# Kernel tuning notes

Hardware: AMD Instinct MI355X
Metric: run time of the kernel (lower is better)

Reference implementation:

```python
import jax, jax.numpy as jnp
import numpy as np


def conv2d(x, w, b):
    # x: [B,C,H,W], w: [O,I,5,5], VALID, stride 1 (matches torch Conv2d defaults)
    y = jax.lax.conv_general_dilated(x, w, (1, 1), 'VALID',
                                     dimension_numbers=('NCHW', 'OIHW', 'NCHW'))
    return y + b[None, :, None, None]


def maxpool_2x5(x):
    # MaxPool2d(kernel=(2,5), stride=(2,1))
    return jax.lax.reduce_window(x, -jnp.inf, jax.lax.max,
                                 (1, 1, 2, 5), (1, 1, 2, 1), 'VALID')


def gru(x, w_ih, w_hh, b_ih, b_hh):
    # Faithful torch nn.GRU (batch_first=False): x is [L, N, 64]; gate order r,z,n.
    H = w_hh.shape[1]
    h0 = jnp.zeros((x.shape[1], H), x.dtype)

    def step(h, xt):
        gi = xt @ w_ih.T + b_ih
        gh = h @ w_hh.T + b_hh
        i_r, i_z, i_n = jnp.split(gi, 3, axis=-1)
        h_r, h_z, h_n = jnp.split(gh, 3, axis=-1)
        r = jax.nn.sigmoid(i_r + h_r)
        z = jax.nn.sigmoid(i_z + h_z)
        n = jnp.tanh(i_n + r * h_n)
        h_new = (1.0 - z) * n + z * h
        return h_new, h_new

    _, ys = jax.lax.scan(step, h0, x)
    return ys


def branch(x, w1, b1, w2, b2, w3, b3, lw, lb, gwih, gwhh, gbih, gbhh):
    x = x[:, None]                      # [B,1,H,W]
    x = conv2d(x, w1, b1)
    x = conv2d(x, w2, b2)
    x = conv2d(x, w3, b3)
    x = maxpool_2x5(x)                  # [B,64,58,W']
    B = x.shape[0]
    x = x.reshape(B, x.shape[-1], 3712)  # same row-major reshape as torch
    x = x @ lw.T + lb                   # [B,W',64]
    # nn.GRU without batch_first scans over dim 0 (batch!) — replicate exactly
    return gru(x, gwih, gwhh, gbih, gbhh)


def _make_params(key):
    ks = iter(jax.random.split(key, 40))
    def p(shape, scale=0.05):
        return (jax.random.normal(next(ks), shape, jnp.float32) * scale)
    d = {}
    for pre in ('e', 't'):
        d[f'{pre}_w1'] = p((16, 1, 5, 5)); d[f'{pre}_b1'] = p((16,))
        d[f'{pre}_w2'] = p((32, 16, 5, 5)); d[f'{pre}_b2'] = p((32,))
        d[f'{pre}_w3'] = p((64, 32, 5, 5)); d[f'{pre}_b3'] = p((64,))
        d[f'{pre}l_w'] = p((64, 3712), 0.01); d[f'{pre}l_b'] = p((64,))
        d[f'{pre}g_wih'] = p((192, 64)); d[f'{pre}g_whh'] = p((192, 64))
        d[f'{pre}g_bih'] = p((192,)); d[f'{pre}g_bhh'] = p((192,))
    d['a_w'] = p((1, 64)); d['a_b'] = p((1,))
    d['h_w'] = p((128, 64)); d['h_b'] = p((128,))
    d['c_w'] = p((2, 128)); d['c_b'] = p((2,))
    return d


def setup_inputs() -> dict:
    key = jax.random.key(0)
    k1, k2, k3 = jax.random.split(key, 3)
    inp = {
        'evaluation': jax.random.normal(k1, (4, 128, 2048), jnp.float32),
        'template': jax.random.normal(k2, (4, 128, 1040), jnp.float32),
    }
    inp.update(_make_params(k3))
    return inp


def reference(evaluation, template,
              e_w1, e_b1, e_w2, e_b2, e_w3, e_b3, el_w, el_b,
              eg_wih, eg_whh, eg_bih, eg_bhh,
              t_w1, t_b1, t_w2, t_b2, t_w3, t_b3, tl_w, tl_b,
              tg_wih, tg_whh, tg_bih, tg_bhh,
              a_w, a_b, h_w, h_b, c_w, c_b):
    e = branch(evaluation, e_w1, e_b1, e_w2, e_b2, e_w3, e_b3,
               el_w, el_b, eg_wih, eg_whh, eg_bih, eg_bhh)   # [B,Se,64]
    t = branch(template, t_w1, t_b1, t_w2, t_b2, t_w3, t_b3,
               tl_w, tl_b, tg_wih, tg_whh, tg_bih, tg_bhh)   # [B,St,64]
    # bmm(template, eval^T) -> [B,St,Se], softmax over Se
    tt = jax.nn.softmax(jnp.einsum('btd,bed->bte', t, e), axis=-1)
    # bmm(tt^T, template) -> [B,Se,64]
    tt = jnp.einsum('bte,btd->bed', tt, t)
    tt = jnp.abs(tt - e)
    # attention over eval sequence positions
    att = jax.nn.softmax((e @ a_w.T + a_b)[..., 0], axis=-1)  # [B,Se]
    # vectorized form of the original Python double loop
    red = jnp.einsum('bed,be->bd', tt, att)                   # [B,64]
    h = jax.nn.relu(red @ h_w.T + h_b)
    return jax.nn.softmax(h @ c_w.T + c_b, axis=-1)           # [B,2]
```

## Files before the change

### kernel.cpp

```cpp
#include <hip/hip_runtime.h>
#include <hip/hip_bf16.h>
#include <cmath>


typedef unsigned short u16;
typedef unsigned int u32;
typedef __attribute__((ext_vector_type(8))) short bf16x8;
typedef __attribute__((ext_vector_type(8))) unsigned short u16x8;
typedef __attribute__((ext_vector_type(16))) float f32x16;

__device__ __forceinline__ u16 f2bf(float f) {
  unsigned int x = __float_as_uint(f);
  return (u16)((x + 0x7fffu + ((x >> 16) & 1u)) >> 16);
}
__device__ __forceinline__ float bf2f(u16 v) {
  return __uint_as_float(((unsigned int)v) << 16);
}
__device__ __forceinline__ u32 f2bf_pk(float a, float b) {
  __hip_bfloat162 h = __float22bfloat162_rn(float2{a, b});
  u32 r;
  __builtin_memcpy(&r, &h, 4);
  return r;
}

static const size_t OFF_BEFF_E  = 0;
static const size_t OFF_BEFF_T  = 64;
static const size_t OFF_BIAS2_E = 128;
static const size_t OFF_BIAS2_T = 320;
static const size_t OFF_WKX_E   = 512;
static const size_t OFF_WKX_T   = 27136;
static const size_t OFF_W12P_E  = 53760;
static const size_t OFF_W12P_T  = 63008;
static const size_t OFF_B12_E   = 72256;
static const size_t OFF_B12_T   = 72288;
static const size_t OFF_LWT1_E  = 72320;
static const size_t OFF_LWT1_T  = 191104;
static const size_t OFF_ATT     = 309888;
static const size_t OFF_XYBF_E  = 318016;
static const size_t OFF_XYBF_T  = 578112;
static const size_t OFF_TTBF    = 709184;
static const size_t OFF_LIN_E   = 840256;
static const size_t OFF_LIN_T   = 1360448;
static const size_t OFF_RED     = 1622592;
static const size_t OFF_RSUM    = 1622848;
static const size_t ZERO_F4     = 196672;
static const size_t ZSTRIDE     = 372;
static const size_t OFF_ATTW    = 1626944;
static const size_t OFF_GI_E    = 2147136;
static const size_t OFF_GI_T    = 3707712;

__global__ __launch_bounds__(320) void prep_kernel(
    const float* __restrict__ w1e, const float* __restrict__ b1e,
    const float* __restrict__ w2e, const float* __restrict__ b2e,
    const float* __restrict__ w1t, const float* __restrict__ b1t,
    const float* __restrict__ w2t, const float* __restrict__ b2t,
    float* __restrict__ w12p_e, float* __restrict__ w12p_t,
    float* __restrict__ b12o_e, float* __restrict__ b12o_t,
    const float* __restrict__ wih_e, const float* __restrict__ bih_e,
    const float* __restrict__ lb_e, float* __restrict__ bias2_e,
    const float* __restrict__ wih_t, const float* __restrict__ bih_t,
    const float* __restrict__ lb_t, float* __restrict__ bias2_t,
    const float* __restrict__ lwe, const float* __restrict__ lwt,
    u16* __restrict__ lwt1_e, u16* __restrict__ lwt1_t,
    float4* __restrict__ zbase) {
  const int bx = blockIdx.x;
  const int tid = threadIdx.x;
  {
    const size_t base = (size_t)bx * ZSTRIDE;
    const float4 z = {0.f, 0.f, 0.f, 0.f};
    for (size_t i = base + tid; i < base + ZSTRIDE && i < ZERO_F4; i += 320)
      zbase[i] = z;
  }
  if (bx >= 66) {
    if (tid < 256) {
      const int k = bx - 66;
      const int br = k / 232, j = k - br * 232;
      const float* src = br ? lwt : lwe;
      u16* dst = br ? lwt1_t : lwt1_e;
      const int e = j * 1024 + tid * 4;
      const int h = e >> 12;
      const int rem = e & 4095;
      const int n = rem >> 6, c = rem & 63;
      const float* s = src + (size_t)n * 3712 + (size_t)c * 58 + h;
      const float v0 = s[0], v1 = s[58], v2 = s[116], v3 = s[174];
      *(u32*)&dst[e] = f2bf_pk(v0, v1);
      *(u32*)&dst[e + 2] = f2bf_pk(v2, v3);
    }
    return;
  }
  if (bx >= 64) {
    const int br = bx - 64;
    const float* wih = br ? wih_t : wih_e;
    const float* bih = br ? bih_t : bih_e;
    const float* lb = br ? lb_t : lb_e;
    float* bias2 = br ? bias2_t : bias2_e;
    __shared__ float s_lb[64];
    if (tid < 64) s_lb[tid] = lb[tid];
    __syncthreads();
    if (tid < 192) {
      float acc = bih[tid];
      const float* wr = wih + tid * 64;
      for (int d = 0; d < 64; ++d) acc = fmaf(wr[d], s_lb[d], acc);
      bias2[tid] = acc;
    }
    return;
  }
  const int br = bx >> 5;
  const float* w1 = br ? w1t : w1e;
  const float* b1 = br ? b1t : b1e;
  const float* w2 = br ? w2t : w2e;
  const float* b2 = br ? b2t : b2e;
  float* w12p = br ? w12p_t : w12p_e;
  float* b12o = br ? b12o_t : b12o_e;
  const int c12 = bx & 31;
  __shared__ float s_w1pad[16 * 169];
  __shared__ float s_w2c[400];
  __shared__ float s_b1[16];
  for (int i = tid; i < 2704; i += 320) s_w1pad[i] = 0.f;
  if (tid < 16) s_b1[tid] = b1[tid];
  __syncthreads();
  for (int i = tid; i < 400; i += 320) {
    const int c1 = i / 25, r = (i % 25) / 5, cc = i % 5;
    s_w1pad[c1 * 169 + (r + 4) * 13 + (cc + 4)] = w1[i];
    s_w2c[i] = w2[c12 * 400 + i];
  }
  __syncthreads();
  if (tid < 289) {
    const int py = tid / 17, px = tid % 17;
    float v = 0.f;
    if (py >= 4 && py <= 12 && px >= 4 && px <= 12) {
      const int sy = py - 4, sx = px - 4;
      float accs[2] = {0.f, 0.f};
// ... 170 lines not shown
#pragma unroll
        for (int ks = 0; ks < 4; ++ks) bb[ks] = *(const bf16x8*)(bp2 + ks * 16);
      }
      f32x16 c0a = {}, c1a = {}, c0b = {}, c1b = {};
      const u16* bxp = s_x + g8;
#pragma unroll
      for (int kx = 0; kx < 6; ++kx) {
        bf16x8 b0 = *(const bf16x8*)(bxp + (l31 + kx) * 24);
        bf16x8 b1 = *(const bf16x8*)(bxp + (32 + l31 + kx) * 24);
        bf16x8 b0q = *(const bf16x8*)(bxp + (l31 + kx + 7) * 24);
        bf16x8 b1q = *(const bf16x8*)(bxp + (32 + l31 + kx + 7) * 24);
        c0a = __builtin_amdgcn_mfma_f32_32x32x16_bf16(wfrag[kx], b0, c0a, 0, 0, 0);
        c1a = __builtin_amdgcn_mfma_f32_32x32x16_bf16(wfrag[kx], b1, c1a, 0, 0, 0);
        c0b = __builtin_amdgcn_mfma_f32_32x32x16_bf16(wfrag[kx + 7], b0q, c0b, 0, 0, 0);
        c1b = __builtin_amdgcn_mfma_f32_32x32x16_bf16(wfrag[kx + 7], b1q, c1b, 0, 0, 0);
      }
      {
        bf16x8 b0 = *(const bf16x8*)(bxp + (l31 + 6) * 24);
        bf16x8 b1 = *(const bf16x8*)(bxp + (32 + l31 + 6) * 24);
        c0a = __builtin_amdgcn_mfma_f32_32x32x16_bf16(wfrag[6], b0, c0a, 0, 0, 0);
        c1a = __builtin_amdgcn_mfma_f32_32x32x16_bf16(wfrag[6], b1, c1a, 0, 0, 0);
      }
#pragma unroll
      for (int r = 0; r < 16; ++r) {
        const int c = cm + (r & 3) + 8 * (r >> 2) + (g8 >> 1);
        u16* o = s_out + (rsel * 64 + c) * 72;
        const u32 pk = f2bf_pk(c0a[r] + c0b[r], c1a[r] + c1b[r]);
        o[l31] = (u16)pk;
        o[32 + l31] = (u16)(pk >> 16);
      }
      __syncthreads();
      {
        const int pc = tid & 63, tg = tid >> 6;
        const int t0 = tg * 16;
        const float bias = s_beff[pc];
        const u16* r0p = s_out + pc * 72 + t0;
        const u16* r1p = s_out + (64 + pc) * 72 + t0;
        const u16x8 a0 = *(const u16x8*)(r0p);
        const u16x8 a1 = *(const u16x8*)(r0p + 8);
        const u16x8 a2 = *(const u16x8*)(r0p + 16);
        const u16x8 q0 = *(const u16x8*)(r1p);
        const u16x8 q1 = *(const u16x8*)(r1p + 8);
        const u16x8 q2 = *(const u16x8*)(r1p + 16);
        float m01[20];
#pragma unroll
        for (int j = 0; j < 8; ++j) {
          m01[j] = fmaxf(bf2f(a0[j]), bf2f(q0[j]));
          m01[j + 8] = fmaxf(bf2f(a1[j]), bf2f(q1[j]));
          if (j < 4) m01[j + 16] = fmaxf(bf2f(a2[j]), bf2f(q2[j]));
        }
#pragma unroll
        for (int i = 0; i < 16; ++i) {
          if (t0 + i < 60) {
            float m = m01[i];
#pragma unroll
            for (int k = 1; k < 5; ++k) m = fmaxf(m, m01[i + k]);
            s_poolT[(t0 + i) * 72 + pc] = f2bf(m + bias);
          }
        }
      }
      __syncthreads();
      {
        const u16* ap2 = s_poolT + (th + l31) * 72 + g8;
#pragma unroll
        for (int ks = 0; ks < 4; ++ks) {
          bf16x8 a = *(const bf16x8*)(ap2 + ks * 16);
          accL = __builtin_amdgcn_mfma_f32_32x32x16_bf16(a, bb[ks], accL, 0, 0, 0);
        }
      }
    }
  }
  {
    const int nn = nh + l31;
#pragma unroll
    for (int r = 0; r < 16; ++r) {
      const int t = th + (r & 3) + 8 * (r >> 2) + (g8 >> 1);
      const int tt = cb + t;
      if (t < 60 && tt < T)
        atomicAdd(&lin[((size_t)b * T + tt) * 64 + nn], accL[r]);
    }
  }
}

__global__ __launch_bounds__(256) void gemm_gi_kernel(
    const float* __restrict__ Ae, const float* __restrict__ Wte,
    const float* __restrict__ biase, float* __restrict__ oute,
    const float* __restrict__ At, const float* __restrict__ Wtt,
    const float* __restrict__ biast, float* __restrict__ outt) {
  const int bx = blockIdx.x;
  const bool ev = bx < 127;
  const float* A = ev ? Ae : At;
  const float* Wt = ev ? Wte : Wtt;
  const float* bias = ev ? biase : biast;
  float* out = ev ? oute : outt;
  const int r0 = (ev ? bx : bx - 127) * 64;
  const int N = 192, K = 64;
  __shared__ float sA[64 * 33];
  __shared__ float sB[64 * 33];
  const int tid = threadIdx.x;
  const int n0 = blockIdx.y * 64;
  const int ty = tid >> 4, tx = tid & 15;
  float acc[4][4] = {};
  for (int kc = 0; kc < K; kc += 32) {
    __syncthreads();
#pragma unroll
    for (int rep = 0; rep < 8; ++rep) {
      const int l = tid + rep * 256;
      const int row = l >> 5, kk = l & 31;
      sA[row * 33 + kk] = A[(size_t)(r0 + row) * K + kc + kk];
      sB[row * 33 + kk] = Wt[(size_t)(n0 + row) * K + kc + kk];
    }
    __syncthreads();
#pragma unroll 8
    for (int kk = 0; kk < 32; ++kk) {
      const float a0 = sA[(ty * 4 + 0) * 33 + kk];
      const float a1 = sA[(ty * 4 + 1) * 33 + kk];
      const float a2 = sA[(ty * 4 + 2) * 33 + kk];
      const float a3 = sA[(ty * 4 + 3) * 33 + kk];
      const float b0 = sB[(tx * 4 + 0) * 33 + kk];
      const float b1 = sB[(tx * 4 + 1) * 33 + kk];
      const float b2 = sB[(tx * 4 + 2) * 33 + kk];
      const float b3 = sB[(tx * 4 + 3) * 33 + kk];
      acc[0][0] = fmaf(a0, b0, acc[0][0]); acc[0][1] = fmaf(a0, b1, acc[0][1]);
      acc[0][2] = fmaf(a0, b2, acc[0][2]); acc[0][3] = fmaf(a0, b3, acc[0][3]);
      acc[1][0] = fmaf(a1, b0, acc[1][0]); acc[1][1] = fmaf(a1, b1, acc[1][1]);
      acc[1][2] = fmaf(a1, b2, acc[1][2]); acc[1][3] = fmaf(a1, b3, acc[1][3]);
      acc[2][0] = fmaf(a2, b0, acc[2][0]); acc[2][1] = fmaf(a2, b1, acc[2][1]);
      acc[2][2] = fmaf(a2, b2, acc[2][2]); acc[2][3] = fmaf(a2, b3, acc[2][3]);
      acc[3][0] = fmaf(a3, b0, acc[3][0]); acc[3][1] = fmaf(a3, b1, acc[3][1]);
      acc[3][2] = fmaf(a3, b2, acc[3][2]); acc[3][3] = fmaf(a3, b3, acc[3][3]);
    }
  }
#pragma unroll
  for (int i = 0; i < 4; ++i)
#pragma unroll
    for (int j = 0; j < 4; ++j)
      out[(size_t)(r0 + ty * 4 + i) * N + n0 + tx * 4 + j] =
          acc[i][j] + bias[n0 + tx * 4 + j];
}

__global__ __launch_bounds__(256) void gru_rec_kernel(
    float* __restrict__ xyE, const float* __restrict__ giE,
    const float* __restrict__ whhE, const float* __restrict__ bhhE,
    float* __restrict__ xyT, const float* __restrict__ giT,
    const float* __restrict__ whhT, const float* __restrict__ bhhT,
    u16* __restrict__ xybfE, u16* __restrict__ xybfT, u16* __restrict__ ttbf,
    const float* __restrict__ a_w, const float* __restrict__ a_b,
    float* __restrict__ logits) {
  const int bxid = blockIdx.x;
  const bool ev = bxid < 127;
  float* xy = ev ? xyE : xyT;
  u16* xybf = ev ? xybfE : xybfT;
  const float* gi = ev ? giE : giT;
  const float* whh = ev ? whhE : whhT;
  const float* bhh = ev ? bhhE : bhhT;
  const int T = ev ? 2032 : 1024;
  const int t0 = (ev ? bxid : bxid - 127) * 16;
  __shared__ float s_whh_t[64 * 192];
  __shared__ float s_h[16][64];
  __shared__ float s_aw[64];
  const int tid = threadIdx.x;
  const int lane = tid & 63, wave = tid >> 6;
  for (int i = tid; i < 192 * 64; i += 256) {
    const int j = i >> 6, d = i & 63;
    s_whh_t[d * 192 + j] = whh[i];
  }
  for (int i = tid; i < 16 * 64; i += 256) (&s_h[0][0])[i] = 0.f;
  if (tid < 64) s_aw[tid] = a_w[tid];
  const float ab = a_b[0];
  const float bhr = bhh[lane], bhz = bhh[64 + lane], bhn = bhh[128 + lane];
  __syncthreads();
  for (int b = 0; b < 4; ++b) {
    float gir[4], giz[4], gin[4];
#pragma unroll
    for (int sl = 0; sl < 4; ++sl) {
      int t = t0 + wave * 4 + sl; if (t > T - 1) t = T - 1;
      const float* girow = gi + ((size_t)b * T + t) * 192;
      gir[sl] = girow[lane]; giz[sl] = girow[64 + lane]; gin[sl] = girow[128 + lane];
    }
    float ahr[4] = {}, ahz[4] = {}, ahn[4] = {};
    for (int d = 0; d < 64; ++d) {
      const float wr_ = s_whh_t[d * 192 + lane];
      const float wz_ = s_whh_t[d * 192 + 64 + lane];
      const float wn_ = s_whh_t[d * 192 + 128 + lane];
#pragma unroll
      for (int sl = 0; sl < 4; ++sl) {
        const float hv = s_h[wave * 4 + sl][d];
        ahr[sl] = fmaf(wr_, hv, ahr[sl]);
        ahz[sl] = fmaf(wz_, hv, ahz[sl]);
        ahn[sl] = fmaf(wn_, hv, ahn[sl]);
      }
    }
    float hn[4];
#pragma unroll
    for (int sl = 0; sl < 4; ++sl) {
      const float r = 1.f / (1.f + __expf(-(gir[sl] + ahr[sl] + bhr)));
      const float z = 1.f / (1.f + __expf(-(giz[sl] + ahz[sl] + bhz)));
      const float n = tanhf(gin[sl] + r * (ahn[sl] + bhn));
      hn[sl] = (1.f - z) * n + z * s_h[wave * 4 + sl][lane];
    }
    __syncthreads();
#pragma unroll
    for (int sl = 0; sl < 4; ++sl) {
      const int t = t0 + wave * 4 + sl;
      s_h[wave * 4 + sl][lane] = hn[sl];
      if (t < T) {
        const size_t idx = ((size_t)b * T + t) * 64 + lane;
        xy[idx] = hn[sl];
        xybf[idx] = f2bf(hn[sl]);
        if (ev) {
          float v = hn[sl] * s_aw[lane];
#pragma unroll
          for (int off = 32; off > 0; off >>= 1) v += __shfl_down(v, off, 64);
          if (lane == 0) logits[b * 2032 + t] = v + ab;
        } else {
          ttbf[((size_t)b * 64 + lane) * 1024 + t] = f2bf(hn[sl]);
        }
      }
    }
    __syncthreads();
  }
}

__global__ __launch_bounds__(256) void rowsum_kernel(
    const u16* __restrict__ tbf, const u16* __restrict__ ebf,
    float* __restrict__ rowsum) {
  __shared__ __align__(16) u16 sA[64 * 72];
  __shared__ __align__(16) u16 sB[128 * 72];
  const int tid = threadIdx.x;
  const int b = blockIdx.z;
  const int tau0 = blockIdx.x * 64;
  const int e0 = blockIdx.y * 128;
  const int lane = tid & 63, wave = tid >> 6;
  const int l31 = lane & 31, g8 = (lane >> 5) * 8;
  {
    const int row = tid >> 2, seg = (tid & 3) * 16;
    const u16* ap = &tbf[((size_t)b * 1024 + tau0 + row) * 64 + seg];
    u16* da = &sA[row * 72 + seg];
    *(u16x8*)da = *(const u16x8*)ap;
    *(u16x8*)(da + 8) = *(const u16x8*)(ap + 8);
  }
#pragma unroll
  for (int r = 0; r < 4; ++r) {
    const int q = tid + r * 256;
    const int row = q >> 3, seg = (q & 7) * 8;
    int eps = e0 + row; if (eps > 2031) eps = 2031;
    *(u16x8*)&sB[row * 72 + seg] =
        *(const u16x8*)&ebf[((size_t)b * 2032 + eps) * 64 + seg];
  }
  __syncthreads();
  const int mh = (wave & 1) * 32;
  const int nq = (wave >> 1) * 64;
  f32x16 acc0 = {}, acc1 = {};
#pragma unroll
  for (int ks = 0; ks < 4; ++ks) {
    bf16x8 a = *(const bf16x8*)&sA[(mh + l31) * 72 + ks * 16 + g8];
    bf16x8 b0 = *(const bf16x8*)&sB[(nq + l31) * 72 + ks * 16 + g8];
    bf16x8 b1 = *(const bf16x8*)&sB[(nq + 32 + l31) * 72 + ks * 16 + g8];
    acc0 = __builtin_amdgcn_mfma_f32_32x32x16_bf16(a, b0, acc0, 0, 0, 0);
    acc1 = __builtin_amdgcn_mfma_f32_32x32x16_bf16(a, b1, acc1, 0, 0, 0);
  }
  const int ep0 = e0 + nq + l31;
  const int ep1 = ep0 + 32;
#pragma unroll
  for (int r = 0; r < 16; ++r) {
    const int tau = tau0 + mh + (r & 3) + 8 * (r >> 2) + (g8 >> 1);
    float part = 0.f;
    if (ep0 < 2032) part += __expf(acc0[r]);
    if (ep1 < 2032) part += __expf(acc1[r]);
#pragma unroll
    for (int off = 16; off > 0; off >>= 1) part += __shfl_down(part, off, 32);
    if (l31 == 0) atomicAdd(&rowsum[b * 1024 + tau], part);
  }
}

__global__ __launch_bounds__(256) void att_softmax_kernel(
    const float* __restrict__ logits, float* __restrict__ attw) {
  __shared__ float s_att[2032];
  __shared__ float sred[4];
  const int tid = threadIdx.x;
  const int lane = tid & 63, wave = tid >> 6;
  const int b = blockIdx.x;
  float m = -3.4e38f;
  for (int i = tid; i < 2032; i += 256) {
    const float v = logits[b * 2032 + i];
    s_att[i] = v;
    m = fmaxf(m, v);
  }
#pragma unroll
  for (int off = 32; off > 0; off >>= 1) m = fmaxf(m, __shfl_down(m, off, 64));
  if (lane == 0) sred[wave] = m;
  __syncthreads();
  m = fmaxf(fmaxf(sred[0], sred[1]), fmaxf(sred[2], sred[3]));
  __syncthreads();
  float ssum = 0.f;
  for (int i = tid; i < 2032; i += 256) {
    const float v = __expf(s_att[i] - m);
    s_att[i] = v;
    ssum += v;
  }
#pragma unroll
  for (int off = 32; off > 0; off >>= 1) ssum += __shfl_down(ssum, off, 64);
  if (lane == 0) sred[wave] = ssum;
  __syncthreads();
  const float inv = 1.f / (sred[0] + sred[1] + sred[2] + sred[3]);
  for (int i = tid; i < 2032; i += 256) attw[b * 2032 + i] = s_att[i] * inv;
}

__global__ __launch_bounds__(256) void pv_red_kernel(
    const u16* __restrict__ tbf, const u16* __restrict__ ebf,
    const u16* __restrict__ ttbf, const float* __restrict__ rowsum,
    const float* __restrict__ attw, const float* __restrict__ emat,
    float* __restrict__ red) {
  __shared__ __align__(16) u16 sE[64 * 72];
  __shared__ __align__(16) u16 sT[64 * 72];
  __shared__ __align__(16) u16 sTT[64 * 72];
  __shared__ __align__(16) u16 sPT[64 * 72];
  __shared__ float s_rs[64];
  __shared__ float s_att[64];
  __shared__ float s_part[4][32];
  const int tid = threadIdx.x;
  const int b = blockIdx.y;
  const int e0 = blockIdx.x * 64;
  const int lane = tid & 63, wave = tid >> 6;
  const int l31 = lane & 31, g8 = (lane >> 5) * 8;
  const int mh = (wave & 1) * 32;
  const int nh = (wave >> 1) * 32;
  {
    const int row = tid >> 2, seg = (tid & 3) * 16;
    int eps = e0 + row; if (eps > 2031) eps = 2031;
    const u16* ap = &ebf[((size_t)b * 2032 + eps) * 64 + seg];
    u16* da = &sE[row * 72 + seg];
    *(u16x8*)da = *(const u16x8*)ap;
    *(u16x8*)(da + 8) = *(const u16x8*)(ap + 8);
  }
  if (tid < 64) {
    const int e = e0 + tid;
    s_att[tid] = (e < 2032) ? attw[b * 2032 + e] : 0.f;
  }
  f32x16 accPV = {};
  for (int ch = 0; ch < 16; ++ch) {
    const int tc = ch * 64;
    __syncthreads();
    {
      const int row = tid >> 2, seg = (tid & 3) * 16;
      const u16* ap = &tbf[((size_t)b * 1024 + tc + row) * 64 + seg];
      u16* da = &sT[row * 72 + seg];
      *(u16x8*)da = *(const u16x8*)ap;
      *(u16x8*)(da + 8) = *(const u16x8*)(ap + 8);
    }
#pragma unroll
    for (int k = 0; k < 2; ++k) {
      const int q = tid + k * 256;
      const int row = q >> 3, seg = (q & 7) * 8;
      *(u16x8*)&sTT[row * 72 + seg] =
          *(const u16x8*)&ttbf[((size_t)b * 64 + row) * 1024 + tc + seg];
    }
    if (tid < 64) s_rs[tid] = 1.0f / rowsum[b * 1024 + tc + tid];
    __syncthreads();
    f32x16 acc = {};
#pragma unroll
    for (int ks = 0; ks < 4; ++ks) {
      bf16x8 a = *(const bf16x8*)&sT[(mh + l31) * 72 + ks * 16 + g8];
      bf16x8 bb = *(const bf16x8*)&sE[(nh + l31) * 72 + ks * 16 + g8];
      acc = __builtin_amdgcn_mfma_f32_32x32x16_bf16(a, bb, acc, 0, 0, 0);
    }
#pragma unroll
    for (int r = 0; r < 16; ++r) {
      const int tl = mh + (r & 3) + 8 * (r >> 2) + (g8 >> 1);
      const int el = nh + l31;
      sPT[el * 72 + tl] = f2bf(__expf(acc[r]) * s_rs[tl]);
    }
    __syncthreads();
#pragma unroll
    for (int ks = 0; ks < 4; ++ks) {
      bf16x8 a = *(const bf16x8*)&sPT[(mh + l31) * 72 + ks * 16 + g8];
      bf16x8 bb = *(const bf16x8*)&sTT[(nh + l31) * 72 + ks * 16 + g8];
      accPV = __builtin_amdgcn_mfma_f32_32x32x16_bf16(a, bb, accPV, 0, 0, 0);
    }
  }
  float local = 0.f;
#pragma unroll
  for (int r = 0; r < 16; ++r) {
    const int el = mh + (r & 3) + 8 * (r >> 2) + (g8 >> 1);
    const int eps = e0 + el;
    if (eps < 2032) {
      const size_t idx = ((size_t)b * 2032 + eps) * 64 + nh + l31;
      local = fmaf(fabsf(accPV[r] - emat[idx]), s_att[el], local);
    }
  }
  local += __shfl_xor(local, 32, 64);
  if (lane < 32) s_part[wave][lane] = local;
  __syncthreads();
  if (tid < 64) {
    const int d = tid;
    const float v = (d < 32) ? (s_part[0][d] + s_part[1][d])
                             : (s_part[2][d - 32] + s_part[3][d - 32]);
    atomicAdd(&red[b * 64 + d], v);
  }
}

__global__ __launch_bounds__(128) void mlp_kernel(
    const float* __restrict__ red, const float* __restrict__ h_w,
    const float* __restrict__ h_b, const float* __restrict__ c_w,
    const float* __restrict__ c_b, float* __restrict__ out) {
  __shared__ float s_red[64];
  __shared__ float s_hv[128];
  const int tid = threadIdx.x;
  const int b = blockIdx.x;
  if (tid < 64) s_red[tid] = red[b * 64 + tid];
  __syncthreads();
  {
    float acc = h_b[tid];
    const float* hw = h_w + tid * 64;
    for (int d = 0; d < 64; ++d) acc = fmaf(s_red[d], hw[d], acc);
    s_hv[tid] = fmaxf(acc, 0.f);
  }
  __syncthreads();
  if (tid == 0) {
    float l0 = c_b[0], l1 = c_b[1];
    for (int j = 0; j < 128; ++j) {
      l0 = fmaf(s_hv[j], c_w[j], l0);
      l1 = fmaf(s_hv[j], c_w[128 + j], l1);
    }
    const float mm = fmaxf(l0, l1);
    const float e0 = __expf(l0 - mm), e1 = __expf(l1 - mm);
    const float invs = 1.f / (e0 + e1);
    out[b * 2 + 0] = e0 * invs;
    out[b * 2 + 1] = e1 * invs;
  }
}

extern "C" void kernel_launch(void* const* d_in, const int* in_sizes, int n_in,
                              void* d_out, int out_size, void* d_ws, size_t ws_size,
                              hipStream_t stream) {
  const float* evaluation = (const float*)d_in[0];
  const float* templ      = (const float*)d_in[1];
  const float* e_w1 = (const float*)d_in[2];
  const float* e_b1 = (const float*)d_in[3];
  const float* e_w2 = (const float*)d_in[4];
  const float* e_b2 = (const float*)d_in[5];
  const float* e_w3 = (const float*)d_in[6];
  const float* e_b3 = (const float*)d_in[7];
  const float* el_w = (const float*)d_in[8];
  const float* el_b = (const float*)d_in[9];
  const float* eg_wih = (const float*)d_in[10];
  const float* eg_whh = (const float*)d_in[11];
  const float* eg_bih = (const float*)d_in[12];
  const float* eg_bhh = (const float*)d_in[13];
  const float* t_w1 = (const float*)d_in[14];
  const float* t_b1 = (const float*)d_in[15];
  const float* t_w2 = (const float*)d_in[16];
  const float* t_b2 = (const float*)d_in[17];
  const float* t_w3 = (const float*)d_in[18];
  const float* t_b3 = (const float*)d_in[19];
  const float* tl_w = (const float*)d_in[20];
  const float* tl_b = (const float*)d_in[21];
  const float* tg_wih = (const float*)d_in[22];
  const float* tg_whh = (const float*)d_in[23];
  const float* tg_bih = (const float*)d_in[24];
  const float* tg_bhh = (const float*)d_in[25];
  const float* a_w = (const float*)d_in[26];
  const float* a_b = (const float*)d_in[27];
  const float* h_w = (const float*)d_in[28];
  const float* h_b = (const float*)d_in[29];
  const float* c_w = (const float*)d_in[30];
  const float* c_b = (const float*)d_in[31];

  float* ws = (float*)d_ws;
  float* beff_e  = ws + OFF_BEFF_E;
  float* beff_t  = ws + OFF_BEFF_T;
  float* bias2_e = ws + OFF_BIAS2_E;
  float* bias2_t = ws + OFF_BIAS2_T;
  u16*   wkx_e   = (u16*)(ws + OFF_WKX_E);
  u16*   wkx_t   = (u16*)(ws + OFF_WKX_T);
  float* w12p_e  = ws + OFF_W12P_E;
  float* w12p_t  = ws + OFF_W12P_T;
  float* b12_e   = ws + OFF_B12_E;
  float* b12_t   = ws + OFF_B12_T;
  u16*   lwt1_e  = (u16*)(ws + OFF_LWT1_E);
  u16*   lwt1_t  = (u16*)(ws + OFF_LWT1_T);
  float* attbuf  = ws + OFF_ATT;
  u16*   xybf_e  = (u16*)(ws + OFF_XYBF_E);
  u16*   xybf_t  = (u16*)(ws + OFF_XYBF_T);
  u16*   ttbf    = (u16*)(ws + OFF_TTBF);
  float* lin_e   = ws + OFF_LIN_E;
  float* lin_t   = ws + OFF_LIN_T;
  float* redbuf  = ws + OFF_RED;
  float* rsum    = ws + OFF_RSUM;
  float* attw    = ws + OFF_ATTW;
  float* gi_e    = ws + OFF_GI_E;
  float* gi_t    = ws + OFF_GI_T;

  prep_kernel<<<530, 320, 0, stream>>>(
      e_w1, e_b1, e_w2, e_b2, t_w1, t_b1, t_w2, t_b2, w12p_e, w12p_t, b12_e, b12_t,
      eg_wih, eg_bih, el_b, bias2_e, tg_wih, tg_bih, tl_b, bias2_t,
      el_w, tl_w, lwt1_e, lwt1_t, (float4*)lin_e);
  compose_weff_kernel<<<dim3(64, 2), 256, 0, stream>>>(
      e_w3, e_b3, t_w3, t_b3, w12p_e, w12p_t, b12_e, b12_t, wkx_e, wkx_t, beff_e, beff_t);

  conv_pool_lin_kernel<<<dim3(34, 10, 8), 256, 0, stream>>>(
      evaluation, wkx_e, beff_e, lwt1_e, lin_e,
      templ, wkx_t, beff_t, lwt1_t, lin_t);
  gemm_gi_kernel<<<dim3(191, 3), 256, 0, stream>>>(
      lin_e, eg_wih, bias2_e, gi_e, lin_t, tg_wih, bias2_t, gi_t);
  gru_rec_kernel<<<191, 256, 0, stream>>>(
      lin_e, gi_e, eg_whh, eg_bhh, lin_t, gi_t, tg_whh, tg_bhh,
      xybf_e, xybf_t, ttbf, a_w, a_b, attbuf);

  rowsum_kernel<<<dim3(16, 16, 4), 256, 0, stream>>>(xybf_t, xybf_e, rsum);
  att_softmax_kernel<<<4, 256, 0, stream>>>(attbuf, attw);
  pv_red_kernel<<<dim3(32, 4), 256, 0, stream>>>(
      xybf_t, xybf_e, ttbf, rsum, attw, lin_e, redbuf);

  mlp_kernel<<<4, 128, 0, stream>>>(redbuf, h_w, h_b, c_w, c_b, (float*)d_out);
}
```

Before: 307.2 us.

## Fuse attention softmax and MLP into pv_red kernel, split D across blocks

Removes the separate attention-softmax and MLP kernels. Each pv_red block recomputes the softmax max and sum over the 2032 logits itself, and the last block to finish (tracked by an atomic counter) runs the final MLP. The grid gains a z dimension that splits the 64 output features into two halves, and the second GEMM's K dimension is split across waves and merged through shared memory. Loads of the next T/TT/rowsum chunk are prefetched into registers. In exchange, every block redundantly reads the full logits row and depends on a zeroed counter in the workspace (ZERO_F4 shifted to cover it).

```diff
diff --git a/kernel.cpp b/kernel.cpp
--- a/kernel.cpp
+++ b/kernel.cpp
@@ -43,9 +43,9 @@
 static const size_t OFF_LIN_T   = 1360448;
 static const size_t OFF_RED     = 1622592;
 static const size_t OFF_RSUM    = 1622848;
-static const size_t ZERO_F4     = 196672;
+static const size_t OFF_CNT     = 1626944;
+static const size_t ZERO_F4     = 196673;
 static const size_t ZSTRIDE     = 372;
-static const size_t OFF_ATTW    = 1626944;
 static const size_t OFF_GI_E    = 2147136;
 static const size_t OFF_GI_T    = 3707712;
 
@@ -576,58 +576,33 @@
   }
 }
 
-__global__ __launch_bounds__(256) void att_softmax_kernel(
-    const float* __restrict__ logits, float* __restrict__ attw) {
-  __shared__ float s_att[2032];
-  __shared__ float sred[4];
-  const int tid = threadIdx.x;
-  const int lane = tid & 63, wave = tid >> 6;
-  const int b = blockIdx.x;
-  float m = -3.4e38f;
-  for (int i = tid; i < 2032; i += 256) {
-    const float v = logits[b * 2032 + i];
-    s_att[i] = v;
-    m = fmaxf(m, v);
-  }
-#pragma unroll
-  for (int off = 32; off > 0; off >>= 1) m = fmaxf(m, __shfl_down(m, off, 64));
-  if (lane == 0) sred[wave] = m;
-  __syncthreads();
-  m = fmaxf(fmaxf(sred[0], sred[1]), fmaxf(sred[2], sred[3]));
-  __syncthreads();
-  float ssum = 0.f;
-  for (int i = tid; i < 2032; i += 256) {
-    const float v = __expf(s_att[i] - m);
-    s_att[i] = v;
-    ssum += v;
-  }
-#pragma unroll
-  for (int off = 32; off > 0; off >>= 1) ssum += __shfl_down(ssum, off, 64);
-  if (lane == 0) sred[wave] = ssum;
-  __syncthreads();
-  const float inv = 1.f / (sred[0] + sred[1] + sred[2] + sred[3]);
-  for (int i = tid; i < 2032; i += 256) attw[b * 2032 + i] = s_att[i] * inv;
-}
-
 __global__ __launch_bounds__(256) void pv_red_kernel(
     const u16* __restrict__ tbf, const u16* __restrict__ ebf,
     const u16* __restrict__ ttbf, const float* __restrict__ rowsum,
-    const float* __restrict__ attw, const float* __restrict__ emat,
-    float* __restrict__ red) {
+    const float* __restrict__ logits, const float* __restrict__ emat,
+    float* __restrict__ red, float* __restrict__ cnt,
+    const float* __restrict__ h_w, const float* __restrict__ h_b,
+    const float* __restrict__ c_w, const float* __restrict__ c_b,
+    float* __restrict__ out) {
   __shared__ __align__(16) u16 sE[64 * 72];
   __shared__ __align__(16) u16 sT[64 * 72];
-  __shared__ __align__(16) u16 sTT[64 * 72];
+  __shared__ __align__(16) u16 sTT[32 * 72];
   __shared__ __align__(16) u16 sPT[64 * 72];
   __shared__ float s_rs[64];
   __shared__ float s_att[64];
-  __shared__ float s_part[4][32];
+  __shared__ float s_red4[4];
+  __shared__ float s_merge[2][32 * 33];
+  __shared__ float s_ep[2][32];
+  __shared__ int s_last;
   const int tid = threadIdx.x;
   const int b = blockIdx.y;
   const int e0 = blockIdx.x * 64;
+  const int dh = blockIdx.z;
   const int lane = tid & 63, wave = tid >> 6;
   const int l31 = lane & 31, g8 = (lane >> 5) * 8;
   const int mh = (wave & 1) * 32;
-  const int nh = (wave >> 1) * 32;
+  const int kh = wave >> 1;
+  const int nh = kh * 32;
   {
     const int row = tid >> 2, seg = (tid & 3) * 16;
     int eps = e0 + row; if (eps > 2031) eps = 2031;
@@ -636,29 +611,57 @@
     *(u16x8*)da = *(const u16x8*)ap;
     *(u16x8*)(da + 8) = *(const u16x8*)(ap + 8);
   }
-  if (tid < 64) {
-    const int e = e0 + tid;
-    s_att[tid] = (e < 2032) ? attw[b * 2032 + e] : 0.f;
+  {
+    float m = -3.4e38f;
+    for (int i = tid; i < 2032; i += 256) m = fmaxf(m, logits[b * 2032 + i]);
+#pragma unroll
+    for (int off = 32; off > 0; off >>= 1) m = fmaxf(m, __shfl_down(m, off, 64));
+    if (lane == 0) s_red4[wave] = m;
+    __syncthreads();
+    m = fmaxf(fmaxf(s_red4[0], s_red4[1]), fmaxf(s_red4[2], s_red4[3]));
+    __syncthreads();
+    float ssum = 0.f;
+    for (int i = tid; i < 2032; i += 256) ssum += __expf(logits[b * 2032 + i] - m);
+#pragma unroll
+    for (int off = 32; off > 0; off >>= 1) ssum += __shfl_down(ssum, off, 64);
+    if (lane == 0) s_red4[wave] = ssum;
+    __syncthreads();
+    const float inv = 1.f / (s_red4[0] + s_red4[1] + s_red4[2] + s_red4[3]);
+    if (tid < 64) {
+      const int e = e0 + tid;
+      s_att[tid] = (e < 2032) ? __expf(logits[b * 2032 + e] - m) * inv : 0.f;
+    }
+  }
+  u16x8 pT0, pT1, pTT;
+  float pRS = 1.f;
+  {
+    const int row = tid >> 2, seg = (tid & 3) * 16;
+    const u16* ap = &tbf[((size_t)b * 1024 + row) * 64 + seg];
+    pT0 = *(const u16x8*)ap; pT1 = *(const u16x8*)(ap + 8);
+    const int r2 = tid >> 3, s2 = (tid & 7) * 8;
+    pTT = *(const u16x8*)&ttbf[((size_t)b * 64 + dh * 32 + r2) * 1024 + s2];
+    if (tid < 64) pRS = rowsum[b * 1024 + tid];
   }
   f32x16 accPV = {};
   for (int ch = 0; ch < 16; ++ch) {
-    const int tc = ch * 64;
     __syncthreads();
     {
       const int row = tid >> 2, seg = (tid & 3) * 16;
+      u16* da = &sT[row * 72 + seg];
+      *(u16x8*)da = pT0; *(u16x8*)(da + 8) = pT1;
+      const int r2 = tid >> 3, s2 = (tid & 7) * 8;
+      *(u16x8*)&sTT[r2 * 72 + s2] = pTT;
+      if (tid < 64) s_rs[tid] = 1.0f / pRS;
+    }
+    if (ch + 1 < 16) {
+      const int tc = (ch + 1) * 64;
+      const int row = tid >> 2, seg = (tid & 3) * 16;
       const u16* ap = &tbf[((size_t)b * 1024 + tc + row) * 64 + seg];
-      u16* da = &sT[row * 72 + seg];
-      *(u16x8*)da = *(const u16x8*)ap;
-      *(u16x8*)(da + 8) = *(const u16x8*)(ap + 8);
-    }
-#pragma unroll
-    for (int k = 0; k < 2; ++k) {
-      const int q = tid + k * 256;
-      const int row = q >> 3, seg = (q & 7) * 8;
-      *(u16x8*)&sTT[row * 72 + seg] =
-          *(const u16x8*)&ttbf[((size_t)b * 64 + row) * 1024 + tc + seg];
-    }
-    if (tid < 64) s_rs[tid] = 1.0f / rowsum[b * 1024 + tc + tid];
+      pT0 = *(const u16x8*)ap; pT1 = *(const u16x8*)(ap + 8);
+      const int r2 = tid >> 3, s2 = (tid & 7) * 8;
+      pTT = *(const u16x8*)&ttbf[((size_t)b * 64 + dh * 32 + r2) * 1024 + tc + s2];
+      if (tid < 64) pRS = rowsum[b * 1024 + tc + tid];
+    }
     __syncthreads();
     f32x16 acc = {};
 #pragma unroll
@@ -675,61 +678,72 @@
     }
     __syncthreads();
 #pragma unroll
-    for (int ks = 0; ks < 4; ++ks) {
+    for (int kq = 0; kq < 2; ++kq) {
+      const int ks = kh * 2 + kq;
       bf16x8 a = *(const bf16x8*)&sPT[(mh + l31) * 72 + ks * 16 + g8];
-      bf16x8 bb = *(const bf16x8*)&sTT[(nh + l31) * 72 + ks * 16 + g8];
+      bf16x8 bb = *(const bf16x8*)&sTT[l31 * 72 + ks * 16 + g8];
       accPV = __builtin_amdgcn_mfma_f32_32x32x16_bf16(a, bb, accPV, 0, 0, 0);
     }
   }
-  float local = 0.f;
-#pragma unroll
-  for (int r = 0; r < 16; ++r) {
-    const int el = mh + (r & 3) + 8 * (r >> 2) + (g8 >> 1);
-    const int eps = e0 + el;
-    if (eps < 2032) {
-      const size_t idx = ((size_t)b * 2032 + eps) * 64 + nh + l31;
-      local = fmaf(fabsf(accPV[r] - emat[idx]), s_att[el], local);
-    }
-  }
-  local += __shfl_xor(local, 32, 64);
-  if (lane < 32) s_part[wave][lane] = local;
   __syncthreads();
-  if (tid < 64) {
-    const int d = tid;
-    const float v = (d < 32) ? (s_part[0][d] + s_part[1][d])
-                             : (s_part[2][d - 32] + s_part[3][d - 32]);
-    atomicAdd(&red[b * 64 + d], v);
-  }
-}
-
-__global__ __launch_bounds__(128) void mlp_kernel(
-    const float* __restrict__ red, const float* __restrict__ h_w,
-    const float* __restrict__ h_b, const float* __restrict__ c_w,
-    const float* __restrict__ c_b, float* __restrict__ out) {
-  __shared__ float s_red[64];
-  __shared__ float s_hv[128];
-  const int tid = threadIdx.x;
-  const int b = blockIdx.x;
-  if (tid < 64) s_red[tid] = red[b * 64 + tid];
+  if (kh == 1) {
+#pragma unroll
+    for (int r = 0; r < 16; ++r) {
+      const int row = (r & 3) + 8 * (r >> 2) + (g8 >> 1);
+      s_merge[wave & 1][row * 33 + l31] = accPV[r];
+    }
+  }
   __syncthreads();
-  {
-    float acc = h_b[tid];
-    const float* hw = h_w + tid * 64;
-    for (int d = 0; d < 64; ++d) acc = fmaf(s_red[d], hw[d], acc);
-    s_hv[tid] = fmaxf(acc, 0.f);
+  if (kh == 0) {
+    float local = 0.f;
+#pragma unroll
+    for (int r = 0; r < 16; ++r) {
+      const int row = (r & 3) + 8 * (r >> 2) + (g8 >> 1);
+      const float pv = accPV[r] + s_merge[wave & 1][row * 33 + l31];
+      const int eps = e0 + mh + row;
+      if (eps < 2032) {
+        const size_t idx = ((size_t)b * 2032 + eps) * 64 + dh * 32 + l31;
+        local = fmaf(fabsf(pv - emat[idx]), s_att[mh + row], local);
+      }
+    }
+    local += __shfl_xor(local, 32, 64);
+    if (lane < 32) s_ep[wave & 1][lane] = local;
   }
   __syncthreads();
+  if (tid < 32)
+    atomicAdd(&red[b * 64 + dh * 32 + tid], s_ep[0][tid] + s_ep[1][tid]);
+  __threadfence();
   if (tid == 0) {
-    float l0 = c_b[0], l1 = c_b[1];
-    for (int j = 0; j < 128; ++j) {
-      l0 = fmaf(s_hv[j], c_w[j], l0);
-      l1 = fmaf(s_hv[j], c_w[128 + j], l1);
-    }
-    const float mm = fmaxf(l0, l1);
-    const float e0 = __expf(l0 - mm), e1 = __expf(l1 - mm);
-    const float invs = 1.f / (e0 + e1);
-    out[b * 2 + 0] = e0 * invs;
-    out[b * 2 + 1] = e1 * invs;
+    const float old = atomicAdd(cnt, 1.0f);
+    s_last = (old > 254.5f) ? 1 : 0;
+  }
+  __syncthreads();
+  if (s_last) {
+    __threadfence();
+    for (int bq = 0; bq < 4; ++bq) {
+      if (tid < 64) s_rs[tid] = red[bq * 64 + tid];
+      __syncthreads();
+      if (tid < 128) {
+        float accq = h_b[tid];
+        const float* hw = h_w + tid * 64;
+        for (int dd = 0; dd < 64; ++dd) accq = fmaf(s_rs[dd], hw[dd], accq);
+        s_merge[0][tid] = fmaxf(accq, 0.f);
+      }
+      __syncthreads();
+      if (tid == 0) {
+        float l0 = c_b[0], l1 = c_b[1];
+        for (int j = 0; j < 128; ++j) {
+          l0 = fmaf(s_merge[0][j], c_w[j], l0);
+          l1 = fmaf(s_merge[0][j], c_w[128 + j], l1);
+        }
+        const float mm = fmaxf(l0, l1);
+        const float e0v = __expf(l0 - mm), e1v = __expf(l1 - mm);
+        const float invs = 1.f / (e0v + e1v);
+        out[bq * 2 + 0] = e0v * invs;
+        out[bq * 2 + 1] = e1v * invs;
+      }
+      __syncthreads();
+    }
   }
 }
 
@@ -790,7 +804,7 @@
   float* lin_t   = ws + OFF_LIN_T;
   float* redbuf  = ws + OFF_RED;
   float* rsum    = ws + OFF_RSUM;
-  float* attw    = ws + OFF_ATTW;
+  float* cntbuf  = ws + OFF_CNT;
   float* gi_e    = ws + OFF_GI_E;
   float* gi_t    = ws + OFF_GI_T;
 
@@ -811,9 +825,7 @@
       xybf_e, xybf_t, ttbf, a_w, a_b, attbuf);
 
   rowsum_kernel<<<dim3(16, 16, 4), 256, 0, stream>>>(xybf_t, xybf_e, rsum);
-  att_softmax_kernel<<<4, 256, 0, stream>>>(attbuf, attw);
-  pv_red_kernel<<<dim3(32, 4), 256, 0, stream>>>(
-      xybf_t, xybf_e, ttbf, rsum, attw, lin_e, redbuf);
-
-  mlp_kernel<<<4, 128, 0, stream>>>(redbuf, h_w, h_b, c_w, c_b, (float*)d_out);
-}
+  pv_red_kernel<<<dim3(32, 4, 2), 256, 0, stream>>>(
+      xybf_t, xybf_e, ttbf, rsum, attbuf, lin_e, redbuf, cntbuf,
+      h_w, h_b, c_w, c_b, (float*)d_out);
+}
```

Measured after the change: 319.3 us. 3.9% more time.

## Fuse GRU input-gate GEMM into the recurrence kernel

Applied to the files above, without the earlier changes.

Removes the separate gemm_gi_kernel and its global gi buffers. The GRU recurrence kernel now stages W_ih and the combined bias in LDS. It loads each step's linear-layer rows into shared memory and accumulates the input gates alongside the hidden-gate dot products in the same d-loop. This saves one launch and the multi-megabyte write and re-read of the gate pre-activations. In exchange, LDS use roughly doubles and the per-step inner loop carries twice the FMA and shared-memory load work.

```diff
diff --git a/kernel.cpp b/kernel.cpp
--- a/kernel.cpp
+++ b/kernel.cpp
@@ -46,8 +46,6 @@
 static const size_t ZERO_F4     = 196672;
 static const size_t ZSTRIDE     = 372;
 static const size_t OFF_ATTW    = 1626944;
-static const size_t OFF_GI_E    = 2147136;
-static const size_t OFF_GI_T    = 3707712;
 
 __global__ __launch_bounds__(320) void prep_kernel(
     const float* __restrict__ w1e, const float* __restrict__ b1e,
@@ -384,68 +382,13 @@
   }
 }
 
-__global__ __launch_bounds__(256) void gemm_gi_kernel(
-    const float* __restrict__ Ae, const float* __restrict__ Wte,
-    const float* __restrict__ biase, float* __restrict__ oute,
-    const float* __restrict__ At, const float* __restrict__ Wtt,
-    const float* __restrict__ biast, float* __restrict__ outt) {
-  const int bx = blockIdx.x;
-  const bool ev = bx < 127;
-  const float* A = ev ? Ae : At;
-  const float* Wt = ev ? Wte : Wtt;
-  const float* bias = ev ? biase : biast;
-  float* out = ev ? oute : outt;
-  const int r0 = (ev ? bx : bx - 127) * 64;
-  const int N = 192, K = 64;
-  __shared__ float sA[64 * 33];
-  __shared__ float sB[64 * 33];
-  const int tid = threadIdx.x;
-  const int n0 = blockIdx.y * 64;
-  const int ty = tid >> 4, tx = tid & 15;
-  float acc[4][4] = {};
-  for (int kc = 0; kc < K; kc += 32) {
-    __syncthreads();
-#pragma unroll
-    for (int rep = 0; rep < 8; ++rep) {
-      const int l = tid + rep * 256;
-      const int row = l >> 5, kk = l & 31;
-      sA[row * 33 + kk] = A[(size_t)(r0 + row) * K + kc + kk];
-      sB[row * 33 + kk] = Wt[(size_t)(n0 + row) * K + kc + kk];
-    }
-    __syncthreads();
-#pragma unroll 8
-    for (int kk = 0; kk < 32; ++kk) {
-      const float a0 = sA[(ty * 4 + 0) * 33 + kk];
-      const float a1 = sA[(ty * 4 + 1) * 33 + kk];
-      const float a2 = sA[(ty * 4 + 2) * 33 + kk];
-      const float a3 = sA[(ty * 4 + 3) * 33 + kk];
-      const float b0 = sB[(tx * 4 + 0) * 33 + kk];
-      const float b1 = sB[(tx * 4 + 1) * 33 + kk];
-      const float b2 = sB[(tx * 4 + 2) * 33 + kk];
-      const float b3 = sB[(tx * 4 + 3) * 33 + kk];
-      acc[0][0] = fmaf(a0, b0, acc[0][0]); acc[0][1] = fmaf(a0, b1, acc[0][1]);
-      acc[0][2] = fmaf(a0, b2, acc[0][2]); acc[0][3] = fmaf(a0, b3, acc[0][3]);
-      acc[1][0] = fmaf(a1, b0, acc[1][0]); acc[1][1] = fmaf(a1, b1, acc[1][1]);
-      acc[1][2] = fmaf(a1, b2, acc[1][2]); acc[1][3] = fmaf(a1, b3, acc[1][3]);
-      acc[2][0] = fmaf(a2, b0, acc[2][0]); acc[2][1] = fmaf(a2, b1, acc[2][1]);
-      acc[2][2] = fmaf(a2, b2, acc[2][2]); acc[2][3] = fmaf(a2, b3, acc[2][3]);
-      acc[3][0] = fmaf(a3, b0, acc[3][0]); acc[3][1] = fmaf(a3, b1, acc[3][1]);
-      acc[3][2] = fmaf(a3, b2, acc[3][2]); acc[3][3] = fmaf(a3, b3, acc[3][3]);
-    }
-  }
-#pragma unroll
-  for (int i = 0; i < 4; ++i)
-#pragma unroll
-    for (int j = 0; j < 4; ++j)
-      out[(size_t)(r0 + ty * 4 + i) * N + n0 + tx * 4 + j] =
-          acc[i][j] + bias[n0 + tx * 4 + j];
-}
-
 __global__ __launch_bounds__(256) void gru_rec_kernel(
-    float* __restrict__ xyE, const float* __restrict__ giE,
-    const float* __restrict__ whhE, const float* __restrict__ bhhE,
-    float* __restrict__ xyT, const float* __restrict__ giT,
-    const float* __restrict__ whhT, const float* __restrict__ bhhT,
+    float* __restrict__ xyE, const float* __restrict__ wihE,
+    const float* __restrict__ bias2E, const float* __restrict__ whhE,
+    const float* __restrict__ bhhE,
+    float* __restrict__ xyT, const float* __restrict__ wihT,
+    const float* __restrict__ bias2T, const float* __restrict__ whhT,
+    const float* __restrict__ bhhT,
     u16* __restrict__ xybfE, u16* __restrict__ xybfT, u16* __restrict__ ttbf,
     const float* __restrict__ a_w, const float* __restrict__ a_b,
     float* __restrict__ logits) {
@@ -453,44 +396,62 @@
   const bool ev = bxid < 127;
   float* xy = ev ? xyE : xyT;
   u16* xybf = ev ? xybfE : xybfT;
-  const float* gi = ev ? giE : giT;
+  const float* wih = ev ? wihE : wihT;
+  const float* b2 = ev ? bias2E : bias2T;
   const float* whh = ev ? whhE : whhT;
   const float* bhh = ev ? bhhE : bhhT;
   const int T = ev ? 2032 : 1024;
   const int t0 = (ev ? bxid : bxid - 127) * 16;
   __shared__ float s_whh_t[64 * 192];
+  __shared__ float s_wih_t[64 * 192];
   __shared__ float s_h[16][64];
+  __shared__ float s_lin[16][64];
   __shared__ float s_aw[64];
+  __shared__ float s_b2[192];
   const int tid = threadIdx.x;
   const int lane = tid & 63, wave = tid >> 6;
   for (int i = tid; i < 192 * 64; i += 256) {
     const int j = i >> 6, d = i & 63;
     s_whh_t[d * 192 + j] = whh[i];
+    s_wih_t[d * 192 + j] = wih[i];
   }
   for (int i = tid; i < 16 * 64; i += 256) (&s_h[0][0])[i] = 0.f;
   if (tid < 64) s_aw[tid] = a_w[tid];
+  if (tid < 192) s_b2[tid] = b2[tid];
   const float ab = a_b[0];
   const float bhr = bhh[lane], bhz = bhh[64 + lane], bhn = bhh[128 + lane];
   __syncthreads();
   for (int b = 0; b < 4; ++b) {
+    for (int i = tid; i < 1024; i += 256) {
+      const int row = i >> 6, d = i & 63;
+      (&s_lin[0][0])[i] = xy[((size_t)b * T + t0 + row) * 64 + d];
+    }
+    __syncthreads();
     float gir[4], giz[4], gin[4];
+    float ahr[4] = {}, ahz[4] = {}, ahn[4] = {};
 #pragma unroll
     for (int sl = 0; sl < 4; ++sl) {
-      int t = t0 + wave * 4 + sl; if (t > T - 1) t = T - 1;
-      const float* girow = gi + ((size_t)b * T + t) * 192;
-      gir[sl] = girow[lane]; giz[sl] = girow[64 + lane]; gin[sl] = girow[128 + lane];
-    }
-    float ahr[4] = {}, ahz[4] = {}, ahn[4] = {};
+      gir[sl] = s_b2[lane];
+      giz[sl] = s_b2[64 + lane];
+      gin[sl] = s_b2[128 + lane];
+    }
     for (int d = 0; d < 64; ++d) {
       const float wr_ = s_whh_t[d * 192 + lane];
       const float wz_ = s_whh_t[d * 192 + 64 + lane];
       const float wn_ = s_whh_t[d * 192 + 128 + lane];
+      const float vr_ = s_wih_t[d * 192 + lane];
+      const float vz_ = s_wih_t[d * 192 + 64 + lane];
+      const float vn_ = s_wih_t[d * 192 + 128 + lane];
 #pragma unroll
       for (int sl = 0; sl < 4; ++sl) {
         const float hv = s_h[wave * 4 + sl][d];
+        const float lv = s_lin[wave * 4 + sl][d];
         ahr[sl] = fmaf(wr_, hv, ahr[sl]);
         ahz[sl] = fmaf(wz_, hv, ahz[sl]);
         ahn[sl] = fmaf(wn_, hv, ahn[sl]);
+        gir[sl] = fmaf(vr_, lv, gir[sl]);
+        giz[sl] = fmaf(vz_, lv, giz[sl]);
+        gin[sl] = fmaf(vn_, lv, gin[sl]);
       }
     }
     float hn[4];
@@ -791,8 +752,6 @@
   float* redbuf  = ws + OFF_RED;
   float* rsum    = ws + OFF_RSUM;
   float* attw    = ws + OFF_ATTW;
-  float* gi_e    = ws + OFF_GI_E;
-  float* gi_t    = ws + OFF_GI_T;
 
   prep_kernel<<<530, 320, 0, stream>>>(
       e_w1, e_b1, e_w2, e_b2, t_w1, t_b1, t_w2, t_b2, w12p_e, w12p_t, b12_e, b12_t,
@@ -804,10 +763,9 @@
   conv_pool_lin_kernel<<<dim3(34, 10, 8), 256, 0, stream>>>(
       evaluation, wkx_e, beff_e, lwt1_e, lin_e,
       templ, wkx_t, beff_t, lwt1_t, lin_t);
-  gemm_gi_kernel<<<dim3(191, 3), 256, 0, stream>>>(
-      lin_e, eg_wih, bias2_e, gi_e, lin_t, tg_wih, bias2_t, gi_t);
   gru_rec_kernel<<<191, 256, 0, stream>>>(
-      lin_e, gi_e, eg_whh, eg_bhh, lin_t, gi_t, tg_whh, tg_bhh,
+      lin_e, eg_wih, bias2_e, eg_whh, eg_bhh,
+      lin_t, tg_wih, bias2_t, tg_whh, tg_bhh,
       xybf_e, xybf_t, ttbf, a_w, a_b, attbuf);
 
   rowsum_kernel<<<dim3(16, 16, 4), 256, 0, stream>>>(xybf_t, xybf_e, rsum);
```

After: 322.4 us. 5.0% more time.

## Fold attention softmax into rowsum launch and MLP tail into pv_red via last-block counter

Applied to the files above, without the earlier changes.

The attention softmax now runs in extra blocks of the rowsum grid, and the final MLP/classifier runs in whichever pv_red block is last to finish, detected with a global atomic counter and thread fences. This removes two separate kernel launches and their launch gaps from the tail of the pipeline. The counter lives in the zeroed workspace region, so the zero-fill bounds were shifted. The cost is a serialized tail in a single block and reliance on fence and atomic ordering across blocks.

```diff
diff --git a/kernel.cpp b/kernel.cpp
--- a/kernel.cpp
+++ b/kernel.cpp
@@ -43,9 +43,10 @@
 static const size_t OFF_LIN_T   = 1360448;
 static const size_t OFF_RED     = 1622592;
 static const size_t OFF_RSUM    = 1622848;
-static const size_t ZERO_F4     = 196672;
+static const size_t OFF_CNT     = 1626944;
+static const size_t ZERO_F4     = 196673;
 static const size_t ZSTRIDE     = 372;
-static const size_t OFF_ATTW    = 1626944;
+static const size_t OFF_ATTW    = 1627072;
 static const size_t OFF_GI_E    = 2147136;
 static const size_t OFF_GI_T    = 3707712;
 
@@ -526,14 +527,45 @@
 
 __global__ __launch_bounds__(256) void rowsum_kernel(
     const u16* __restrict__ tbf, const u16* __restrict__ ebf,
-    float* __restrict__ rowsum) {
+    float* __restrict__ rowsum,
+    const float* __restrict__ logits, float* __restrict__ attw) {
+  const int tid = threadIdx.x;
+  const int b = blockIdx.z;
+  const int lane = tid & 63, wave = tid >> 6;
+  if (blockIdx.x == 16) {
+    if (blockIdx.y != 0) return;
+    __shared__ float s_att[2032];
+    __shared__ float sred[4];
+    float m = -3.4e38f;
+    for (int i = tid; i < 2032; i += 256) {
+      const float v = logits[b * 2032 + i];
+      s_att[i] = v;
+      m = fmaxf(m, v);
+    }
+#pragma unroll
+    for (int off = 32; off > 0; off >>= 1) m = fmaxf(m, __shfl_down(m, off, 64));
+    if (lane == 0) sred[wave] = m;
+    __syncthreads();
+    m = fmaxf(fmaxf(sred[0], sred[1]), fmaxf(sred[2], sred[3]));
+    __syncthreads();
+    float ssum = 0.f;
+    for (int i = tid; i < 2032; i += 256) {
+      const float v = __expf(s_att[i] - m);
+      s_att[i] = v;
+      ssum += v;
+    }
+#pragma unroll
+    for (int off = 32; off > 0; off >>= 1) ssum += __shfl_down(ssum, off, 64);
+    if (lane == 0) sred[wave] = ssum;
+    __syncthreads();
+    const float inv = 1.f / (sred[0] + sred[1] + sred[2] + sred[3]);
+    for (int i = tid; i < 2032; i += 256) attw[b * 2032 + i] = s_att[i] * inv;
+    return;
+  }
   __shared__ __align__(16) u16 sA[64 * 72];
   __shared__ __align__(16) u16 sB[128 * 72];
-  const int tid = threadIdx.x;
-  const int b = blockIdx.z;
   const int tau0 = blockIdx.x * 64;
   const int e0 = blockIdx.y * 128;
-  const int lane = tid & 63, wave = tid >> 6;
   const int l31 = lane & 31, g8 = (lane >> 5) * 8;
   {
     const int row = tid >> 2, seg = (tid & 3) * 16;
@@ -576,44 +608,14 @@
   }
 }
 
-__global__ __launch_bounds__(256) void att_softmax_kernel(
-    const float* __restrict__ logits, float* __restrict__ attw) {
-  __shared__ float s_att[2032];
-  __shared__ float sred[4];
-  const int tid = threadIdx.x;
-  const int lane = tid & 63, wave = tid >> 6;
-  const int b = blockIdx.x;
-  float m = -3.4e38f;
-  for (int i = tid; i < 2032; i += 256) {
-    const float v = logits[b * 2032 + i];
-    s_att[i] = v;
-    m = fmaxf(m, v);
-  }
-#pragma unroll
-  for (int off = 32; off > 0; off >>= 1) m = fmaxf(m, __shfl_down(m, off, 64));
-  if (lane == 0) sred[wave] = m;
-  __syncthreads();
-  m = fmaxf(fmaxf(sred[0], sred[1]), fmaxf(sred[2], sred[3]));
-  __syncthreads();
-  float ssum = 0.f;
-  for (int i = tid; i < 2032; i += 256) {
-    const float v = __expf(s_att[i] - m);
-    s_att[i] = v;
-    ssum += v;
-  }
-#pragma unroll
-  for (int off = 32; off > 0; off >>= 1) ssum += __shfl_down(ssum, off, 64);
-  if (lane == 0) sred[wave] = ssum;
-  __syncthreads();
-  const float inv = 1.f / (sred[0] + sred[1] + sred[2] + sred[3]);
-  for (int i = tid; i < 2032; i += 256) attw[b * 2032 + i] = s_att[i] * inv;
-}
-
 __global__ __launch_bounds__(256) void pv_red_kernel(
     const u16* __restrict__ tbf, const u16* __restrict__ ebf,
     const u16* __restrict__ ttbf, const float* __restrict__ rowsum,
     const float* __restrict__ attw, const float* __restrict__ emat,
-    float* __restrict__ red) {
+    float* __restrict__ red, float* __restrict__ cnt,
+    const float* __restrict__ h_w, const float* __restrict__ h_b,
+    const float* __restrict__ c_w, const float* __restrict__ c_b,
+    float* __restrict__ out) {
   __shared__ __align__(16) u16 sE[64 * 72];
   __shared__ __align__(16) u16 sT[64 * 72];
   __shared__ __align__(16) u16 sTT[64 * 72];
@@ -621,6 +623,7 @@
   __shared__ float s_rs[64];
   __shared__ float s_att[64];
   __shared__ float s_part[4][32];
+  __shared__ int s_last;
   const int tid = threadIdx.x;
   const int b = blockIdx.y;
   const int e0 = blockIdx.x * 64;
@@ -700,36 +703,39 @@
                              : (s_part[2][d - 32] + s_part[3][d - 32]);
     atomicAdd(&red[b * 64 + d], v);
   }
-}
-
-__global__ __launch_bounds__(128) void mlp_kernel(
-    const float* __restrict__ red, const float* __restrict__ h_w,
-    const float* __restrict__ h_b, const float* __restrict__ c_w,
-    const float* __restrict__ c_b, float* __restrict__ out) {
-  __shared__ float s_red[64];
-  __shared__ float s_hv[128];
-  const int tid = threadIdx.x;
-  const int b = blockIdx.x;
-  if (tid < 64) s_red[tid] = red[b * 64 + tid];
+  __threadfence();
+  if (tid == 0) {
+    const float old = atomicAdd(cnt, 1.0f);
+    s_last = (old > 126.5f) ? 1 : 0;
+  }
   __syncthreads();
-  {
-    float acc = h_b[tid];
-    const float* hw = h_w + tid * 64;
-    for (int d = 0; d < 64; ++d) acc = fmaf(s_red[d], hw[d], acc);
-    s_hv[tid] = fmaxf(acc, 0.f);
-  }
-  __syncthreads();
-  if (tid == 0) {
-    float l0 = c_b[0], l1 = c_b[1];
-    for (int j = 0; j < 128; ++j) {
-      l0 = fmaf(s_hv[j], c_w[j], l0);
-      l1 = fmaf(s_hv[j], c_w[128 + j], l1);
-    }
-    const float mm = fmaxf(l0, l1);
-    const float e0 = __expf(l0 - mm), e1 = __expf(l1 - mm);
-    const float invs = 1.f / (e0 + e1);
-    out[b * 2 + 0] = e0 * invs;
-    out[b * 2 + 1] = e1 * invs;
+  if (s_last) {
+    __threadfence();
+    float* s_hv = &s_part[0][0];
+    for (int bq = 0; bq < 4; ++bq) {
+      if (tid < 64) s_rs[tid] = red[bq * 64 + tid];
+      __syncthreads();
+      if (tid < 128) {
+        float accq = h_b[tid];
+        const float* hw = h_w + tid * 64;
+        for (int dd = 0; dd < 64; ++dd) accq = fmaf(s_rs[dd], hw[dd], accq);
+        s_hv[tid] = fmaxf(accq, 0.f);
+      }
+      __syncthreads();
+      if (tid == 0) {
+        float l0 = c_b[0], l1 = c_b[1];
+        for (int j = 0; j < 128; ++j) {
+          l0 = fmaf(s_hv[j], c_w[j], l0);
+          l1 = fmaf(s_hv[j], c_w[128 + j], l1);
+        }
+        const float mm = fmaxf(l0, l1);
+        const float e0v = __expf(l0 - mm), e1v = __expf(l1 - mm);
+        const float invs = 1.f / (e0v + e1v);
+        out[bq * 2 + 0] = e0v * invs;
+        out[bq * 2 + 1] = e1v * invs;
+      }
+      __syncthreads();
+    }
   }
 }
 
@@ -790,6 +796,7 @@
   float* lin_t   = ws + OFF_LIN_T;
   float* redbuf  = ws + OFF_RED;
   float* rsum    = ws + OFF_RSUM;
+  float* cntbuf  = ws + OFF_CNT;
   float* attw    = ws + OFF_ATTW;
   float* gi_e    = ws + OFF_GI_E;
   float* gi_t    = ws + OFF_GI_T;
@@ -810,10 +817,9 @@
       lin_e, gi_e, eg_whh, eg_bhh, lin_t, gi_t, tg_whh, tg_bhh,
       xybf_e, xybf_t, ttbf, a_w, a_b, attbuf);
 
-  rowsum_kernel<<<dim3(16, 16, 4), 256, 0, stream>>>(xybf_t, xybf_e, rsum);
-  att_softmax_kernel<<<4, 256, 0, stream>>>(attbuf, attw);
+  rowsum_kernel<<<dim3(17, 16, 4), 256, 0, stream>>>(
+      xybf_t, xybf_e, rsum, attbuf, attw);
   pv_red_kernel<<<dim3(32, 4), 256, 0, stream>>>(
-      xybf_t, xybf_e, ttbf, rsum, attw, lin_e, redbuf);
-
-  mlp_kernel<<<4, 128, 0, stream>>>(redbuf, h_w, h_b, c_w, c_b, (float*)d_out);
-}
+      xybf_t, xybf_e, ttbf, rsum, attw, lin_e, redbuf, cntbuf,
+      h_w, h_b, c_w, c_b, (float*)d_out);
+}
```

Measured after the change: 323.1 us. 1.05x slower.
